# Performance work log

Hardware: AMD Instinct MI355X
Metric: run time of the kernel (lower is better)

Reference implementation:

```python
import jax, jax.numpy as jnp
import numpy as np

E = 1_000_000   # edges (temporal neighbor facts)
D = 128         # emb_dim
N = 200_000     # nodes carrying hidden state
B = 512         # queries (batch)
R = 240         # num_rel -> rel table has 2R+1 rows
T = 100_000     # tail nodes (scatter output size)


def setup_inputs() -> dict:
    key = jax.random.key(0)
    ks = jax.random.split(key, 14)
    b_col  = jax.random.randint(ks[0], (E,), 0, B)
    n_col  = jax.random.randint(ks[1], (E,), 0, N)
    h_col  = jax.random.randint(ks[2], (E,), 0, N)
    r_col  = jax.random.randint(ks[3], (E,), 0, 2 * R)   # r+1 in [1, 2R]
    t_col  = jax.random.randint(ks[4], (E,), 0, N)
    ts_col = jax.random.randint(ks[5], (E,), 0, 1000)
    facts = jnp.stack([b_col, n_col, h_col, r_col, t_col, ts_col], axis=1)
    s = 1.0 / np.sqrt(D)
    return {
        "hidden":     jax.random.normal(ks[6], (N, D), jnp.float32) * 0.02,
        "rel_table":  jax.random.normal(ks[7], (2 * R + 1, D), jnp.float32) * 0.02,
        "Ws":         jax.random.normal(ks[8], (D, D), jnp.float32) * s,
        "Wr":         jax.random.normal(ks[9], (D, D), jnp.float32) * s,
        "Wqr_w":      jax.random.normal(ks[10], (D, D), jnp.float32) * s,
        "Wqr_b":      jnp.zeros((D,), jnp.float32),
        "wa_w":       jax.random.normal(ks[11], (D, 1), jnp.float32) * s,
        "wa_b":       jnp.zeros((1,), jnp.float32),
        "Wh":         jax.random.normal(ks[12], (D, D), jnp.float32) * s,
        "query_rel":  jax.random.randint(ks[13], (B,), 0, 2 * R),
        "facts":      facts,
        "tail_index": jax.random.randint(jax.random.fold_in(key, 99), (E,), 0, T),
        "tail_nodes": jnp.arange(T),
    }


def reference(hidden, rel_table, Ws, Wr, Wqr_w, Wqr_b, wa_w, wa_b, Wh,
              query_rel, facts, tail_index, tail_nodes):
    b = facts[:, 0]
    n = facts[:, 1]
    r = facts[:, 3]
    h_e = hidden[n]                      # [E, D] gather node hidden
    hr  = rel_table[r + 1]               # [E, D] gather relation emb
    q_r = rel_table[query_rel + 1][b]    # [E, D] per-edge query relation
    # attention MLP: sigmoid(w_alpha(relu(Ws h + Wr r + Wqr q + b)))
    pre = h_e @ Ws + hr @ Wr + (q_r @ Wqr_w + Wqr_b)          # [E, D]
    alpha = jax.nn.sigmoid(jax.nn.relu(pre) @ wa_w + wa_b)    # [E, 1]
    message = alpha * (h_e + hr)                              # [E, D]
    agg = jax.ops.segment_sum(message, tail_index,
                              num_segments=tail_nodes.shape[0])  # [T, D]
    return agg @ Wh                      # act = identity (default)
```

## Files before the change

### kernel.cpp

```cpp
#include <hip/hip_runtime.h>
#include <hip/hip_fp16.h>
#include <math.h>

#define DD 128
#define CAP 64

typedef _Float16 half_t;
typedef __attribute__((ext_vector_type(8))) _Float16 half8;
typedef __attribute__((ext_vector_type(4))) float floatx4;

#define LDW 136

__device__ __forceinline__ __half2 relu2(__half2 x) {
    return __hmul2(x, __hgt2(x, __float2half2_rn(0.f)));
}

template <int CTRL>
__device__ __forceinline__ float dpp_add(float x) {
    int y = __builtin_amdgcn_update_dpp(0, __float_as_int(x), CTRL, 0xf, 0xf, true);
    return x + __int_as_float(y);
}

__global__ void wt4(const float* __restrict__ W0, const float* __restrict__ W1,
                    const float* __restrict__ W2, const float* __restrict__ W3,
                    half_t* __restrict__ T0, half_t* __restrict__ T1,
                    half_t* __restrict__ T2, half_t* __restrict__ T3) {
    const float* W = blockIdx.x == 0 ? W0 : blockIdx.x == 1 ? W1 : blockIdx.x == 2 ? W2 : W3;
    half_t* T      = blockIdx.x == 0 ? T0 : blockIdx.x == 1 ? T1 : blockIdx.x == 2 ? T2 : T3;
    for (int i = threadIdx.x; i < DD * DD; i += blockDim.x) {
        int n = i >> 7, k = i & 127;
        T[i] = (half_t)W[(size_t)k * DD + n];
    }
}

__global__ __launch_bounds__(256) void gemm_mfma(
    const float* __restrict__ table, const int* __restrict__ idx, int idxAdd, int M,
    const half_t* __restrict__ WT_g, const float* __restrict__ bias,
    float* __restrict__ OutF, __half* __restrict__ OutH) {
    __shared__ half_t WT[DD * LDW];
    __shared__ half_t As[64 * LDW];
    int tid = threadIdx.x;
    int lane = tid & 63;
    int w = tid >> 6;
    int rowf = lane & 15;
    int kgrp = (lane >> 4) * 8;

    for (int i = tid; i < 2048; i += 256) {
        int n = i >> 4, ch = i & 15;
        *(half8*)(WT + n * LDW + ch * 8) = *(const half8*)(WT_g + n * DD + ch * 8);
    }
    int tileM = blockIdx.x * 64;
    for (int i = tid; i < 2048; i += 256) {
        int row = i >> 5, c4 = i & 31;
        int gr = tileM + row;
        float4 v = make_float4(0.f, 0.f, 0.f, 0.f);
        if (gr < M) {
            int src = idx ? (idx[gr] + idxAdd) : gr;
            v = *(const float4*)(table + (size_t)src * DD + c4 * 4);
        }
        __half2 h01 = __floats2half2_rn(v.x, v.y);
        __half2 h23 = __floats2half2_rn(v.z, v.w);
        *(uint2*)(As + row * LDW + c4 * 4) = make_uint2(*(unsigned*)&h01, *(unsigned*)&h23);
    }
    __syncthreads();

    floatx4 acc[8];
#pragma unroll
    for (int t = 0; t < 8; t++) acc[t] = (floatx4){0.f, 0.f, 0.f, 0.f};
    const half_t* ap = As + (w * 16 + rowf) * LDW + kgrp;
    const half_t* bp0 = WT + rowf * LDW + kgrp;
#pragma unroll
    for (int kk = 0; kk < DD; kk += 32) {
        half8 a = *(const half8*)(ap + kk);
#pragma unroll
        for (int t = 0; t < 8; t++) {
            half8 b = *(const half8*)(bp0 + t * 16 * LDW + kk);
            acc[t] = __builtin_amdgcn_mfma_f32_16x16x32_f16(a, b, acc[t], 0, 0, 0);
        }
    }
    int orow = tileM + w * 16 + (lane >> 4) * 4;
#pragma unroll
    for (int t = 0; t < 8; t++) {
        int col = t * 16 + rowf;
        float bv = bias ? bias[col] : 0.f;
#pragma unroll
        for (int i = 0; i < 4; i++) {
            int gr = orow + i;
            if (gr < M) {
                float o = acc[t][i] + bv;
                if (OutF) OutF[(size_t)gr * DD + col] = o;
                if (OutH) OutH[(size_t)gr * DD + col] = __float2half(o);
            }
        }
    }
}

__global__ __launch_bounds__(256) void gemm_pack_mfma(
    const float* __restrict__ table, int M,
    const half_t* __restrict__ WT_g, __half* __restrict__ Packed) {
    __shared__ half_t WT[DD * LDW];
    __shared__ half_t As[64 * LDW];
    int tid = threadIdx.x;
    int lane = tid & 63;
    int w = tid >> 6;
    int rowf = lane & 15;
    int kgrp = (lane >> 4) * 8;

    for (int i = tid; i < 2048; i += 256) {
        int n = i >> 4, ch = i & 15;
        *(half8*)(WT + n * LDW + ch * 8) = *(const half8*)(WT_g + n * DD + ch * 8);
    }
    int tileM = blockIdx.x * 64;
    for (int i = tid; i < 2048; i += 256) {
        int row = i >> 5, c4 = i & 31;
        int gr = tileM + row;
        float4 v = make_float4(0.f, 0.f, 0.f, 0.f);
        if (gr < M) v = *(const float4*)(table + (size_t)gr * DD + c4 * 4);
        __half2 h01 = __floats2half2_rn(v.x, v.y);
        __half2 h23 = __floats2half2_rn(v.z, v.w);
        uint2 u = make_uint2(*(unsigned*)&h01, *(unsigned*)&h23);
        *(uint2*)(As + row * LDW + c4 * 4) = u;
        if (gr < M) *(uint2*)(Packed + (size_t)gr * 256 + c4 * 4) = u;
    }
    __syncthreads();

    floatx4 acc[8];
#pragma unroll
    for (int t = 0; t < 8; t++) acc[t] = (floatx4){0.f, 0.f, 0.f, 0.f};
    const half_t* ap = As + (w * 16 + rowf) * LDW + kgrp;
    const half_t* bp0 = WT + rowf * LDW + kgrp;
#pragma unroll
    for (int kk = 0; kk < DD; kk += 32) {
        half8 a = *(const half8*)(ap + kk);
#pragma unroll
        for (int t = 0; t < 8; t++) {
            half8 b = *(const half8*)(bp0 + t * 16 * LDW + kk);
            acc[t] = __builtin_amdgcn_mfma_f32_16x16x32_f16(a, b, acc[t], 0, 0, 0);
        }
    }
    int orow = tileM + w * 16 + (lane >> 4) * 4;
#pragma unroll
    for (int t = 0; t < 8; t++) {
        int col = t * 16 + rowf;
#pragma unroll
        for (int i = 0; i < 4; i++) {
            int gr = orow + i;
            if (gr < M) Packed[(size_t)gr * 256 + 128 + col] = __float2half(acc[t][i]);
        }
    }
}

__global__ __launch_bounds__(256) void alpha_kernel(
    const __half* __restrict__ HB, const __half* __restrict__ RB,
    const __half* __restrict__ QB, const int* __restrict__ facts,
    const float* __restrict__ wa, const float* __restrict__ wa_b,
    __half* __restrict__ alphaH, int E) {
    int tid = threadIdx.x;
    int lane = tid & 63;
    int wv = blockIdx.x * 4 + (tid >> 6);
    int e = wv * 2 + (lane >> 5);
    bool valid = e < E;
    int ec = valid ? e : (E - 1);
    int c = (lane & 31) * 4;

    int2 bn = *(const int2*)(facts + ec * 6);
    int r = facts[ec * 6 + 3];
    int b_ = bn.x, n_ = bn.y;

    uint2 hu = *(const uint2*)(HB + n_ * 256 + 128 + c);
    uint2 ru = *(const uint2*)(RB + (r + 1) * 256 + 128 + c);
    uint2 qu = *(const uint2*)(QB + b_ * DD + c);
    __half2 h2a = *(__half2*)&hu.x, h2b = *(__half2*)&hu.y;
    __half2 r2a = *(__half2*)&ru.x, r2b = *(__half2*)&ru.y;
    __half2 q2a = *(__half2*)&qu.x, q2b = *(__half2*)&qu.y;

    float4 wv4 = *(const float4*)(wa + c);
    __half2 wa2a = __halves2half2(__float2half(wv4.x), __float2half(wv4.y));
    __half2 wa2b = __halves2half2(__float2half(wv4.z), __float2half(wv4.w));

    __half2 p2a = relu2(__hadd2(__hadd2(h2a, r2a), q2a));
    __half2 p2b = relu2(__hadd2(__hadd2(h2b, r2b), q2b));
    __half2 t2 = __hfma2(p2a, wa2a, __hmul2(p2b, wa2b));
    float t = __half2float(__low2half(t2)) + __half2float(__high2half(t2));

    t = dpp_add<0x111>(t);
    t = dpp_add<0x112>(t);
    t = dpp_add<0x114>(t);
    t = dpp_add<0x118>(t);
    t = dpp_add<0x142>(t);

    float al = 1.f / (1.f + __expf(-(t + wa_b[0])));
    if (((lane & 31) == 31) && valid) alphaH[e] = __float2half(al);
}

__global__ void scatter_kernel(const int* __restrict__ facts, const int* __restrict__ tail,
                               const __half* __restrict__ alphaH,
                               int* __restrict__ cursor, int2* __restrict__ meta, int E) {
    int e = blockIdx.x * blockDim.x + threadIdx.x;
    if (e >= E) return;
    int n = facts[e * 6 + 1];
    int r = facts[e * 6 + 3];
    int t = tail[e];
    unsigned ab = __half_as_ushort(alphaH[e]);
    int slot = atomicAdd(&cursor[t], 1);
    if (slot < CAP) meta[(size_t)t * CAP + slot] = make_int2(n, (r + 1) | (int)(ab << 16));
}

__global__ __launch_bounds__(256) void agg_lite(
    const __half* __restrict__ HB, const __half* __restrict__ RB,
    const int2* __restrict__ meta, const int* __restrict__ cursor,
    float* __restrict__ agg, int T) {
    int w = threadIdx.x >> 6;
    int lane = threadIdx.x & 63;
    int seg = blockIdx.x * 4 + w;
    if (seg >= T) return;
    int cnt = cursor[seg];
    if (cnt > CAP) cnt = CAP;
    const int2* mp = meta + seg * CAP;
    int co = lane * 2;
    __half2 acc = __float2half2_rn(0.f);

#define FB(m)                                                                  \
    {                                                                          \
        int n_ = (m).x;                                                        \
        int rr = (m).y & 0xFFFF;                                               \
        __half al = __ushort_as_half((unsigned short)((unsigned)(m).y >> 16)); \
        unsigned hu = *(const unsigned*)(HB + n_ * 256 + co);                  \
        unsigned ru = *(const unsigned*)(RB + rr * 256 + co);                  \
        __half2 s = __hadd2(*(__half2*)&hu, *(__half2*)&ru);                   \
        acc = __hfma2(__half2half2(al), s, acc);                               \
    }

    int i = 0;
    for (; i + 1 < cnt; i += 2) {
        int2 m0 = mp[i];
        int2 m1 = mp[i + 1];
        FB(m0);
        FB(m1);
    }
    if (i < cnt) {
        int2 m0 = mp[i];
        FB(m0);
    }
#undef FB

    float2 o;
    o.x = __half2float(__low2half(acc));
    o.y = __half2float(__high2half(acc));
    *(float2*)(agg + seg * DD + co) = o;
}

extern "C" void kernel_launch(void* const* d_in, const int* in_sizes, int n_in,
                              void* d_out, int out_size, void* d_ws, size_t ws_size,
                              hipStream_t stream) {
    const float* hidden    = (const float*)d_in[0];
    const float* rel_table = (const float*)d_in[1];
    const float* Ws        = (const float*)d_in[2];
    const float* Wr        = (const float*)d_in[3];
    const float* Wqr_w     = (const float*)d_in[4];
    const float* Wqr_b     = (const float*)d_in[5];
    const float* wa_w      = (const float*)d_in[6];
    const float* wa_b      = (const float*)d_in[7];
    const float* Wh        = (const float*)d_in[8];
    const int* query_rel   = (const int*)d_in[9];
    const int* facts       = (const int*)d_in[10];
    const int* tail_index  = (const int*)d_in[11];

    int N     = in_sizes[0] / DD;
    int Rrows = in_sizes[1] / DD;
    int B     = in_sizes[9];
    int E     = in_sizes[11];
    int T     = in_sizes[12];

    char* ws = (char*)d_ws;
    size_t off = 0;
    auto alloc = [&](size_t bytes) -> void* {
        void* p = ws + off;
        off += (bytes + 255) & ~(size_t)255;
        return p;
    };
    __half* HB  = (__half*)alloc((size_t)N * 256 * 2);
    __half* RB  = (__half*)alloc((size_t)Rrows * 256 * 2);
    __half* QB  = (__half*)alloc((size_t)B * DD * 2);
    int* cursor = (int*)alloc((size_t)T * 4);
    int2* meta  = (int2*)alloc((size_t)T * CAP * 8);
    float* agg  = (float*)alloc((size_t)T * DD * 4);
    half_t* WsT  = (half_t*)alloc((size_t)DD * DD * 2);
    half_t* WrT  = (half_t*)alloc((size_t)DD * DD * 2);
    half_t* WqrT = (half_t*)alloc((size_t)DD * DD * 2);
    half_t* WhT  = (half_t*)alloc((size_t)DD * DD * 2);
    __half* alphaH = (__half*)alloc((size_t)E * 2);

    (void)hipMemsetAsync(cursor, 0, (size_t)T * 4, stream);

    wt4<<<4, 256, 0, stream>>>(Ws, Wr, Wqr_w, Wh, WsT, WrT, WqrT, WhT);

    gemm_pack_mfma<<<(N + 63) / 64, 256, 0, stream>>>(hidden, N, WsT, HB);
    gemm_pack_mfma<<<(Rrows + 63) / 64, 256, 0, stream>>>(rel_table, Rrows, WrT, RB);
    gemm_mfma<<<(B + 63) / 64, 256, 0, stream>>>(rel_table, query_rel, 1, B,
                                                 WqrT, Wqr_b, nullptr, QB);

    alpha_kernel<<<(E + 7) / 8, 256, 0, stream>>>(HB, RB, QB, facts, wa_w, wa_b,
                                                  alphaH, E);

    scatter_kernel<<<(E + 255) / 256, 256, 0, stream>>>(facts, tail_index, alphaH,
                                                        cursor, meta, E);

    agg_lite<<<(T + 3) / 4, 256, 0, stream>>>(HB, RB, meta, cursor, agg, T);

    gemm_mfma<<<(T + 63) / 64, 256, 0, stream>>>(agg, nullptr, 0, T, WhT, nullptr,
                                                 (float*)d_out, nullptr);
}
```

Before: 517.6 us.

## Fuse alpha computation into scatter kernel and unroll aggregation gathers with fp32 accumulation

Merges the alpha kernel and the scatter kernel into one launch, so alpha is computed per edge and written straight into the per-tail meta bucket. This drops the alphaH intermediate buffer and one kernel launch. Each 16-lane group now handles one edge with 8-wide half loads, and each wave processes 8 edges instead of 2. The aggregation loop reads meta four entries at a time with vector loads to issue more independent gathers, and accumulates in fp32 instead of half2. That changes numerics slightly but should be more accurate.

```diff
diff --git a/kernel.cpp b/kernel.cpp
--- a/kernel.cpp
+++ b/kernel.cpp
@@ -150,60 +150,87 @@
     }
 }
 
-__global__ __launch_bounds__(256) void alpha_kernel(
+__global__ __launch_bounds__(256) void alpha_scatter(
     const __half* __restrict__ HB, const __half* __restrict__ RB,
     const __half* __restrict__ QB, const int* __restrict__ facts,
-    const float* __restrict__ wa, const float* __restrict__ wa_b,
-    __half* __restrict__ alphaH, int E) {
+    const int* __restrict__ tail, const float* __restrict__ wa,
+    const float* __restrict__ wa_b,
+    int* __restrict__ cursor, int2* __restrict__ meta, int E) {
     int tid = threadIdx.x;
     int lane = tid & 63;
-    int wv = blockIdx.x * 4 + (tid >> 6);
-    int e = wv * 2 + (lane >> 5);
-    bool valid = e < E;
-    int ec = valid ? e : (E - 1);
-    int c = (lane & 31) * 4;
-
-    int2 bn = *(const int2*)(facts + ec * 6);
-    int r = facts[ec * 6 + 3];
-    int b_ = bn.x, n_ = bn.y;
-
-    uint2 hu = *(const uint2*)(HB + n_ * 256 + 128 + c);
-    uint2 ru = *(const uint2*)(RB + (r + 1) * 256 + 128 + c);
-    uint2 qu = *(const uint2*)(QB + b_ * DD + c);
-    __half2 h2a = *(__half2*)&hu.x, h2b = *(__half2*)&hu.y;
-    __half2 r2a = *(__half2*)&ru.x, r2b = *(__half2*)&ru.y;
-    __half2 q2a = *(__half2*)&qu.x, q2b = *(__half2*)&qu.y;
-
-    float4 wv4 = *(const float4*)(wa + c);
-    __half2 wa2a = __halves2half2(__float2half(wv4.x), __float2half(wv4.y));
-    __half2 wa2b = __halves2half2(__float2half(wv4.z), __float2half(wv4.w));
-
-    __half2 p2a = relu2(__hadd2(__hadd2(h2a, r2a), q2a));
-    __half2 p2b = relu2(__hadd2(__hadd2(h2b, r2b), q2b));
-    __half2 t2 = __hfma2(p2a, wa2a, __hmul2(p2b, wa2b));
-    float t = __half2float(__low2half(t2)) + __half2float(__high2half(t2));
-
-    t = dpp_add<0x111>(t);
-    t = dpp_add<0x112>(t);
-    t = dpp_add<0x114>(t);
-    t = dpp_add<0x118>(t);
-    t = dpp_add<0x142>(t);
-
-    float al = 1.f / (1.f + __expf(-(t + wa_b[0])));
-    if (((lane & 31) == 31) && valid) alphaH[e] = __float2half(al);
-}
-
-__global__ void scatter_kernel(const int* __restrict__ facts, const int* __restrict__ tail,
-                               const __half* __restrict__ alphaH,
-                               int* __restrict__ cursor, int2* __restrict__ meta, int E) {
-    int e = blockIdx.x * blockDim.x + threadIdx.x;
-    if (e >= E) return;
-    int n = facts[e * 6 + 1];
-    int r = facts[e * 6 + 3];
-    int t = tail[e];
-    unsigned ab = __half_as_ushort(alphaH[e]);
-    int slot = atomicAdd(&cursor[t], 1);
-    if (slot < CAP) meta[(size_t)t * CAP + slot] = make_int2(n, (r + 1) | (int)(ab << 16));
+    int g = lane >> 4;
+    int cl = lane & 15;
+    int c = cl * 8;
+    int wv = (blockIdx.x * 256 + tid) >> 6;
+    int e0 = wv * 8 + g;
+
+    float4 wva = *(const float4*)(wa + c);
+    float4 wvb = *(const float4*)(wa + c + 4);
+    __half2 w0 = __halves2half2(__float2half(wva.x), __float2half(wva.y));
+    __half2 w1 = __halves2half2(__float2half(wva.z), __float2half(wva.w));
+    __half2 w2 = __halves2half2(__float2half(wvb.x), __float2half(wvb.y));
+    __half2 w3 = __halves2half2(__float2half(wvb.z), __float2half(wvb.w));
+    float wb = wa_b[0];
+
+    int f0 = e0, f1 = e0 + 4;
+    bool v0 = f0 < E, v1 = f1 < E;
+    int fc0 = v0 ? f0 : 0, fc1 = v1 ? f1 : 0;
+
+    int2 bn0 = *(const int2*)(facts + (size_t)fc0 * 6);
+    int r0 = facts[(size_t)fc0 * 6 + 3];
+    int tl0 = tail[fc0];
+    int2 bn1 = *(const int2*)(facts + (size_t)fc1 * 6);
+    int r1 = facts[(size_t)fc1 * 6 + 3];
+    int tl1 = tail[fc1];
+
+    uint4 h0 = *(const uint4*)(HB + (size_t)bn0.y * 256 + 128 + c);
+    uint4 rr0 = *(const uint4*)(RB + (size_t)(r0 + 1) * 256 + 128 + c);
+    uint4 q0 = *(const uint4*)(QB + (size_t)bn0.x * DD + c);
+    uint4 h1 = *(const uint4*)(HB + (size_t)bn1.y * 256 + 128 + c);
+    uint4 rr1 = *(const uint4*)(RB + (size_t)(r1 + 1) * 256 + 128 + c);
+    uint4 q1 = *(const uint4*)(QB + (size_t)bn1.x * DD + c);
+
+#define DOT8(hu, ru, qu, out)                                                          \
+    {                                                                                  \
+        __half2 p0 = relu2(__hadd2(__hadd2(*(__half2*)&(hu).x, *(__half2*)&(ru).x),    \
+                                   *(__half2*)&(qu).x));                               \
+        __half2 p1 = relu2(__hadd2(__hadd2(*(__half2*)&(hu).y, *(__half2*)&(ru).y),    \
+                                   *(__half2*)&(qu).y));                               \
+        __half2 p2 = relu2(__hadd2(__hadd2(*(__half2*)&(hu).z, *(__half2*)&(ru).z),    \
+                                   *(__half2*)&(qu).z));                               \
+        __half2 p3 = relu2(__hadd2(__hadd2(*(__half2*)&(hu).w, *(__half2*)&(ru).w),    \
+                                   *(__half2*)&(qu).w));                               \
+        __half2 t2 = __hfma2(p1, w1, __hmul2(p0, w0));                                 \
+        t2 = __hfma2(p2, w2, t2);                                                      \
+        t2 = __hfma2(p3, w3, t2);                                                      \
+        out = __half2float(__low2half(t2)) + __half2float(__high2half(t2));            \
+    }
+    float t0, t1;
+    DOT8(h0, rr0, q0, t0);
+    DOT8(h1, rr1, q1, t1);
+#undef DOT8
+
+    t0 = dpp_add<0x111>(t0); t0 = dpp_add<0x112>(t0);
+    t0 = dpp_add<0x114>(t0); t0 = dpp_add<0x118>(t0);
+    t1 = dpp_add<0x111>(t1); t1 = dpp_add<0x112>(t1);
+    t1 = dpp_add<0x114>(t1); t1 = dpp_add<0x118>(t1);
+
+    if (cl == 15) {
+        float a0 = 1.f / (1.f + __expf(-(t0 + wb)));
+        float a1 = 1.f / (1.f + __expf(-(t1 + wb)));
+        unsigned ab0 = (unsigned)__half_as_ushort(__float2half(a0));
+        unsigned ab1 = (unsigned)__half_as_ushort(__float2half(a1));
+        if (v0) {
+            int slot = atomicAdd(&cursor[tl0], 1);
+            if (slot < CAP)
+                meta[(size_t)tl0 * CAP + slot] = make_int2(bn0.y, (r0 + 1) | (int)(ab0 << 16));
+        }
+        if (v1) {
+            int slot = atomicAdd(&cursor[tl1], 1);
+            if (slot < CAP)
+                meta[(size_t)tl1 * CAP + slot] = make_int2(bn1.y, (r1 + 1) | (int)(ab1 << 16));
+        }
+    }
 }
 
 __global__ __launch_bounds__(256) void agg_lite(
@@ -216,38 +243,46 @@
     if (seg >= T) return;
     int cnt = cursor[seg];
     if (cnt > CAP) cnt = CAP;
-    const int2* mp = meta + seg * CAP;
+    const int2* mp = meta + (size_t)seg * CAP;
     int co = lane * 2;
-    __half2 acc = __float2half2_rn(0.f);
-
-#define FB(m)                                                                  \
+    float ax = 0.f, ay = 0.f;
+
+#define ACC(hu, ru, y_)                                                        \
     {                                                                          \
-        int n_ = (m).x;                                                        \
-        int rr = (m).y & 0xFFFF;                                               \
-        __half al = __ushort_as_half((unsigned short)((unsigned)(m).y >> 16)); \
-        unsigned hu = *(const unsigned*)(HB + n_ * 256 + co);                  \
-        unsigned ru = *(const unsigned*)(RB + rr * 256 + co);                  \
-        __half2 s = __hadd2(*(__half2*)&hu, *(__half2*)&ru);                   \
-        acc = __hfma2(__half2half2(al), s, acc);                               \
+        __half2 s = __hadd2(*(__half2*)&(hu), *(__half2*)&(ru));               \
+        float al =                                                             \
+            __half2float(__ushort_as_half((unsigned short)((unsigned)(y_) >> 16))); \
+        float2 sf = __half22float2(s);                                         \
+        ax = fmaf(al, sf.x, ax);                                               \
+        ay = fmaf(al, sf.y, ay);                                               \
     }
 
     int i = 0;
-    for (; i + 1 < cnt; i += 2) {
-        int2 m0 = mp[i];
-        int2 m1 = mp[i + 1];
-        FB(m0);
-        FB(m1);
-    }
-    if (i < cnt) {
-        int2 m0 = mp[i];
-        FB(m0);
-    }
-#undef FB
-
-    float2 o;
-    o.x = __half2float(__low2half(acc));
-    o.y = __half2float(__high2half(acc));
-    *(float2*)(agg + seg * DD + co) = o;
+    for (; i + 3 < cnt; i += 4) {
+        int4 ma = *(const int4*)(mp + i);
+        int4 mb = *(const int4*)(mp + i + 2);
+        unsigned h0 = *(const unsigned*)(HB + (size_t)ma.x * 256 + co);
+        unsigned r0 = *(const unsigned*)(RB + (size_t)(ma.y & 0xFFFF) * 256 + co);
+        unsigned h1 = *(const unsigned*)(HB + (size_t)ma.z * 256 + co);
+        unsigned r1 = *(const unsigned*)(RB + (size_t)(ma.w & 0xFFFF) * 256 + co);
+        unsigned h2 = *(const unsigned*)(HB + (size_t)mb.x * 256 + co);
+        unsigned r2 = *(const unsigned*)(RB + (size_t)(mb.y & 0xFFFF) * 256 + co);
+        unsigned h3 = *(const unsigned*)(HB + (size_t)mb.z * 256 + co);
+        unsigned r3 = *(const unsigned*)(RB + (size_t)(mb.w & 0xFFFF) * 256 + co);
+        ACC(h0, r0, ma.y);
+        ACC(h1, r1, ma.w);
+        ACC(h2, r2, mb.y);
+        ACC(h3, r3, mb.w);
+    }
+    for (; i < cnt; i++) {
+        int2 m = mp[i];
+        unsigned hu = *(const unsigned*)(HB + (size_t)m.x * 256 + co);
+        unsigned ru = *(const unsigned*)(RB + (size_t)(m.y & 0xFFFF) * 256 + co);
+        ACC(hu, ru, m.y);
+    }
+#undef ACC
+
+    *(float2*)(agg + (size_t)seg * DD + co) = make_float2(ax, ay);
 }
 
 extern "C" void kernel_launch(void* const* d_in, const int* in_sizes, int n_in,
@@ -289,7 +324,6 @@
     half_t* WrT  = (half_t*)alloc((size_t)DD * DD * 2);
     half_t* WqrT = (half_t*)alloc((size_t)DD * DD * 2);
     half_t* WhT  = (half_t*)alloc((size_t)DD * DD * 2);
-    __half* alphaH = (__half*)alloc((size_t)E * 2);
 
     (void)hipMemsetAsync(cursor, 0, (size_t)T * 4, stream);
 
@@ -300,11 +334,8 @@
     gemm_mfma<<<(B + 63) / 64, 256, 0, stream>>>(rel_table, query_rel, 1, B,
                                                  WqrT, Wqr_b, nullptr, QB);
 
-    alpha_kernel<<<(E + 7) / 8, 256, 0, stream>>>(HB, RB, QB, facts, wa_w, wa_b,
-                                                  alphaH, E);
-
-    scatter_kernel<<<(E + 255) / 256, 256, 0, stream>>>(facts, tail_index, alphaH,
-                                                        cursor, meta, E);
+    alpha_scatter<<<(E + 31) / 32, 256, 0, stream>>>(HB, RB, QB, facts, tail_index,
+                                                     wa_w, wa_b, cursor, meta, E);
 
     agg_lite<<<(T + 3) / 4, 256, 0, stream>>>(HB, RB, meta, cursor, agg, T);
 
```

Result: faster. 472.3 us (-8.8%).
